# Kernel tuning notes

Measured on AMD Instinct MI355X. Metric: run time of the kernel, lower is better.

Reference implementation:

```python
import jax, jax.numpy as jnp
import numpy as np
import math

D_MODEL = 1024
N_HEADS = 16
D_HEAD = D_MODEL // N_HEADS
EPS = 1e-5


def layer_norm(x, w, b):
    mu = jnp.mean(x, axis=-1, keepdims=True)
    var = jnp.mean(jnp.square(x - mu), axis=-1, keepdims=True)
    return (x - mu) * jax.lax.rsqrt(var + EPS) * w + b


def setup_inputs() -> dict:
    key = jax.random.key(0)
    ks = jax.random.split(key, 8)
    b, n, d = 1, 4096, D_MODEL
    s = 0.02
    return {
        "x": jax.random.normal(ks[0], (b, n, d), dtype=jnp.float32),
        "ln1_w": jnp.ones((d,), jnp.float32),
        "ln1_b": jnp.zeros((d,), jnp.float32),
        "ln2_w": jnp.ones((d,), jnp.float32),
        "ln2_b": jnp.zeros((d,), jnp.float32),
        "w_qkv": jax.random.normal(ks[1], (d, 3 * d), jnp.float32) * s,  # [in, out]
        "w_o": jax.random.normal(ks[2], (d, d), jnp.float32) * s,
        "w_ff1": jax.random.normal(ks[3], (d, 4 * d), jnp.float32) * s,
        "b_ff1": jnp.zeros((4 * d,), jnp.float32),
        "w_ff2": jax.random.normal(ks[4], (4 * d, d), jnp.float32) * s,
        "b_ff2": jnp.zeros((d,), jnp.float32),
    }


def reference(x, ln1_w, ln1_b, ln2_w, ln2_b, w_qkv, w_o, w_ff1, b_ff1, w_ff2, b_ff2):
    b, n, d = x.shape
    # --- attention sub-block ---
    h = layer_norm(x, ln1_w, ln1_b)
    qkv = (h @ w_qkv).reshape(b, n, 3, N_HEADS, D_HEAD)
    q, k, v = qkv[:, :, 0], qkv[:, :, 1], qkv[:, :, 2]  # [b, n, h, dh]
    scale = 1.0 / math.sqrt(D_HEAD)
    s = jnp.einsum("bqhd,bkhd->bhqk", q, k) * scale  # materialized [b,h,n,n]
    causal = jnp.tril(jnp.ones((n, n), dtype=bool))
    s = jnp.where(causal, s, -jnp.inf)
    a = jax.nn.softmax(s, axis=-1)
    out = jnp.einsum("bhqk,bkhd->bqhd", a, v).reshape(b, n, d)
    x = x + out @ w_o
    # --- FFN sub-block ---
    h2 = layer_norm(x, ln2_w, ln2_b)
    ff = jax.nn.gelu(h2 @ w_ff1 + b_ff1, approximate=False) @ w_ff2 + b_ff2
    return x + ff
```

## Files before the change

kernel.cpp:

```cpp
#include <hip/hip_runtime.h>
#include <hip/hip_bf16.h>
#include <cstdint>
#include <cstddef>

typedef __attribute__((ext_vector_type(8))) __bf16 bf16x8;
typedef __attribute__((ext_vector_type(4))) __bf16 bf16x4;
typedef __attribute__((ext_vector_type(4))) float f32x4;
typedef __attribute__((ext_vector_type(16))) float f32x16;
typedef __attribute__((ext_vector_type(4))) unsigned int uint4v;

#define MFMA16(a, b, c) __builtin_amdgcn_mfma_f32_16x16x32_bf16(a, b, c, 0, 0, 0)
#define MFMA32(a, b, c) __builtin_amdgcn_mfma_f32_32x32x16_bf16(a, b, c, 0, 0, 0)

__device__ __forceinline__ void gload_lds16(const void* g, void* l) {
  __builtin_amdgcn_global_load_lds(
      (__attribute__((address_space(1))) uint32_t*)g,
      (__attribute__((address_space(3))) uint32_t*)l,
      16, 0, 0);
}

__device__ __forceinline__ unsigned pkbf(float a, float b) {
  unsigned short x = __builtin_bit_cast(unsigned short, (__bf16)a);
  unsigned short y = __builtin_bit_cast(unsigned short, (__bf16)b);
  return (unsigned)x | ((unsigned)y << 16);
}

__device__ __forceinline__ float fexp2(float x) {
  float r;
  asm("v_exp_f32 %0, %1" : "=v"(r) : "v"(x));
  return r;
}

__global__ __launch_bounds__(256) void pre_kernel(
    const float* __restrict__ w_qkv, __bf16* __restrict__ wqkvT,
    const float* __restrict__ x, const float* __restrict__ ln1_w,
    const float* __restrict__ ln1_b, __bf16* __restrict__ h) {
  __shared__ float sm[32 * 33];
  int bid = blockIdx.x;
  int tx = threadIdx.x, ty = threadIdx.y;
  if (bid < 3072) {
    int bx = bid % 96, by = bid / 96;
    int gcol = bx * 32 + tx;
#pragma unroll
    for (int j = 0; j < 4; j++) {
      int grow = by * 32 + ty + j * 8;
      sm[(ty + j * 8) * 33 + tx] = w_qkv[(size_t)grow * 3072 + gcol];
    }
    __syncthreads();
#pragma unroll
    for (int j = 0; j < 4; j++) {
      int n = bx * 32 + ty + j * 8;
      wqkvT[(size_t)n * 1024 + by * 32 + tx] = (__bf16)sm[tx * 33 + ty + j * 8];
    }
    return;
  }
  int row = bid - 3072;
  int t = ty * 32 + tx;
  const float4* xr = (const float4*)(x + (size_t)row * 1024);
  float4 v = xr[t];
  float s = v.x + v.y + v.z + v.w;
  float sq = v.x * v.x + v.y * v.y + v.z * v.z + v.w * v.w;
#pragma unroll
  for (int m = 1; m < 64; m <<= 1) {
    s += __shfl_xor(s, m);
    sq += __shfl_xor(sq, m);
  }
  float* rs = sm;
  float* rq = sm + 4;
  int wid = t >> 6;
  if ((t & 63) == 0) { rs[wid] = s; rq[wid] = sq; }
  __syncthreads();
  s = rs[0] + rs[1] + rs[2] + rs[3];
  sq = rq[0] + rq[1] + rq[2] + rq[3];
  float mean = s * (1.0f / 1024.0f);
  float var = sq * (1.0f / 1024.0f) - mean * mean;
  float rstd = rsqrtf(var + 1e-5f);
  float4 wv = ((const float4*)ln1_w)[t];
  float4 bv = ((const float4*)ln1_b)[t];
  bf16x4 o;
  o[0] = (__bf16)((v.x - mean) * rstd * wv.x + bv.x);
  o[1] = (__bf16)((v.y - mean) * rstd * wv.y + bv.y);
  o[2] = (__bf16)((v.z - mean) * rstd * wv.z + bv.z);
  o[3] = (__bf16)((v.w - mean) * rstd * wv.w + bv.w);
  *(bf16x4*)(h + (size_t)row * 1024 + t * 4) = o;
}

__global__ __launch_bounds__(256, 2) void gemm_splitk128_kernel(
    const __bf16* __restrict__ A, const __bf16* __restrict__ BT,
    int M, int N, int K, int kchunk, __bf16* __restrict__ P) {
  __shared__ __bf16 lsA[128 * 64];
  __shared__ __bf16 lsB[128 * 64];
  int t = threadIdx.x;
  int m0 = blockIdx.y * 128, n0 = blockIdx.x * 128;
  int kbase = blockIdx.z * kchunk;
  __bf16* pout = P + (size_t)blockIdx.z * M * N;
  int wid = t >> 6, lane = t & 63, lo = lane & 15, g = lane >> 4;
  int wr = wid >> 1, wc = wid & 1;
  f32x4 acc[4][4] = {};
  const __bf16* ag = A + (size_t)(m0 + (t >> 3)) * K + (t & 7) * 8;
  const __bf16* bg = BT + (size_t)(n0 + (t >> 3)) * K + (t & 7) * 8;
  for (int k0 = kbase; k0 < kbase + kchunk; k0 += 64) {
#pragma unroll
    for (int i = 0; i < 4; i++) {
      gload_lds16(ag + (size_t)i * 32 * K + k0, &lsA[i * 2048 + t * 8]);
      gload_lds16(bg + (size_t)i * 32 * K + k0, &lsB[i * 2048 + t * 8]);
    }
    __syncthreads();
#pragma unroll
    for (int kk = 0; kk < 2; kk++) {
      bf16x8 af[4], bfr[4];
#pragma unroll
      for (int mi = 0; mi < 4; mi++)
        af[mi] = *(const bf16x8*)&lsA[(wr * 64 + mi * 16 + lo) * 64 + kk * 32 + g * 8];
#pragma unroll
      for (int ni = 0; ni < 4; ni++)
        bfr[ni] = *(const bf16x8*)&lsB[(wc * 64 + ni * 16 + lo) * 64 + kk * 32 + g * 8];
#pragma unroll
      for (int mi = 0; mi < 4; mi++)
#pragma unroll
        for (int ni = 0; ni < 4; ni++)
          acc[mi][ni] = MFMA16(af[mi], bfr[ni], acc[mi][ni]);
    }
    __syncthreads();
  }
#pragma unroll
  for (int mi = 0; mi < 4; mi++) {
#pragma unroll
    for (int ni = 0; ni < 4; ni++) {
      int col = n0 + wc * 64 + ni * 16 + lo;
      int row0 = m0 + wr * 64 + mi * 16 + g * 4;
#pragma unroll
      for (int r = 0; r < 4; r++)
        pout[(size_t)(row0 + r) * N + col] = (__bf16)acc[mi][ni][r];
    }
  }
}

__global__ __launch_bounds__(256) void out_reduce_ln_kernel(
    const __bf16* __restrict__ p0, const __bf16* __restrict__ p1,
    const float* __restrict__ x, const float* __restrict__ w,
    const float* __restrict__ b, float* __restrict__ x2,
    __bf16* __restrict__ h) {
  int row = blockIdx.x, t = threadIdx.x;
  size_t base = (size_t)row * 1024 + t * 4;
  bf16x4 a = *(const bf16x4*)&p0[base];
  bf16x4 b4 = *(const bf16x4*)&p1[base];
  float4 xv = *(const float4*)&x[base];
  float4 v;
  v.x = xv.x + (float)a[0] + (float)b4[0];
  v.y = xv.y + (float)a[1] + (float)b4[1];
  v.z = xv.z + (float)a[2] + (float)b4[2];
  v.w = xv.w + (float)a[3] + (float)b4[3];
  *(float4*)&x2[base] = v;
  float s = v.x + v.y + v.z + v.w;
  float sq = v.x * v.x + v.y * v.y + v.z * v.z + v.w * v.w;
#pragma unroll
  for (int m = 1; m < 64; m <<= 1) {
    s += __shfl_xor(s, m);
    sq += __shfl_xor(sq, m);
  }
  __shared__ float rs[4], rq[4];
  int wid = t >> 6;
  if ((t & 63) == 0) { rs[wid] = s; rq[wid] = sq; }
  __syncthreads();
  s = rs[0] + rs[1] + rs[2] + rs[3];
  sq = rq[0] + rq[1] + rq[2] + rq[3];
  float mean = s * (1.0f / 1024.0f);
  float var = sq * (1.0f / 1024.0f) - mean * mean;
  float rstd = rsqrtf(var + 1e-5f);
  float4 wv = ((const float4*)w)[t];
  float4 bv = ((const float4*)b)[t];
  bf16x4 o;
  o[0] = (__bf16)((v.x - mean) * rstd * wv.x + bv.x);
  o[1] = (__bf16)((v.y - mean) * rstd * wv.y + bv.y);
  o[2] = (__bf16)((v.z - mean) * rstd * wv.z + bv.z);
  o[3] = (__bf16)((v.w - mean) * rstd * wv.w + bv.w);
  *(bf16x4*)&h[base] = o;
}

template <int EPI>
__global__ __launch_bounds__(512, 2) void gemm256_kernel(
    const __bf16* __restrict__ A, const __bf16* __restrict__ BT,
    int M, int N, int K, int nkc,
    const float* __restrict__ bias, __bf16* __restrict__ outb,
    __bf16* __restrict__ P0, __bf16* __restrict__ P1,
    __bf16* __restrict__ P2, __bf16* __restrict__ P3) {
  __shared__ __bf16 lsA[2][2][128 * 64];
  __shared__ __bf16 lsB[2][2][128 * 64];
  int nbx = N >> 8;
  int nwg = (M >> 8) * nbx;
  int bid = blockIdx.x;
  int swz = (bid & 7) * (nwg >> 3) + (bid >> 3);
  int m0 = (swz / nbx) << 8, n0 = (swz % nbx) << 8;
  int kc = blockIdx.y;
  int kt0 = kc * nkc;
  int t = threadIdx.x;
  int wid = t >> 6, lane = t & 63, lo = lane & 15, g = lane >> 4;
  int wm = wid >> 2, wn = wid & 3;
  int srow = t >> 3, sgrp = t & 7;

  auto stA = [&](int d, int h, int kt) {
#pragma unroll
    for (int i = 0; i < 2; i++) {
      int row = i * 64 + srow;
      int gs = (sgrp ^ (row & 7)) * 8;
      gload_lds16(A + (size_t)(m0 + h * 128 + row) * K + kt * 64 + gs,
                  &lsA[d][h][(i * 512 + t) * 8]);
    }
  };
  auto stB = [&](int d, int h, int kt) {
#pragma unroll
    for (int i = 0; i < 2; i++) {
      int row = i * 64 + srow;
      int gs = (sgrp ^ (row & 7)) * 8;
      gload_lds16(BT + (size_t)(n0 + h * 128 + row) * K + kt * 64 + gs,
                  &lsB[d][h][(i * 512 + t) * 8]);
    }
  };
  auto rdA = [&](int d, int f, int kk) -> bf16x8 {
    int row = (f & 3) * 32 + wm * 16 + lo;
    return *(const bf16x8*)&lsA[d][f >> 2][row * 64 + (((kk * 4 + g) ^ (lo & 7)) * 8)];
  };
  auto rdB = [&](int d, int ni, int kk) -> bf16x8 {
    int row = (ni & 1) * 64 + wn * 16 + lo;
    return *(const bf16x8*)&lsB[d][ni >> 1][row * 64 + (((kk * 4 + g) ^ (lo & 7)) * 8)];
  };

  f32x4 acc[8][4] = {};
  stA(0, 0, kt0); stB(0, 0, kt0); stB(0, 1, kt0); stA(0, 1, kt0);
  asm volatile("s_waitcnt vmcnt(4)" ::: "memory");
  __builtin_amdgcn_s_barrier();

  for (int ki = 0; ki < nkc; ki++) {
    int kt = kt0 + ki;
    int d = ki & 1, nx = d ^ 1;
    bool pf = (ki + 1) < nkc;
    bf16x8 fa[4][2], fb0[2][2], fb1[2][2];
#pragma unroll
    for (int f = 0; f < 4; f++) { fa[f][0] = rdA(d, f, 0); fa[f][1] = rdA(d, f, 1); }
#pragma unroll
    for (int n = 0; n < 2; n++) { fb0[n][0] = rdB(d, n, 0); fb0[n][1] = rdB(d, n, 1); }
    if (pf) { stA(nx, 0, kt + 1); stB(nx, 0, kt + 1); }
    __builtin_amdgcn_s_barrier();
    __builtin_amdgcn_s_setprio(1);
#pragma unroll
    for (int f = 0; f < 4; f++)
#pragma unroll
      for (int n = 0; n < 2; n++) {
        acc[f][n] = MFMA16(fa[f][0], fb0[n][0], acc[f][n]);
        acc[f][n] = MFMA16(fa[f][1], fb0[n][1], acc[f][n]);
      }
    __builtin_amdgcn_s_setprio(0);
    asm volatile("s_waitcnt vmcnt(6)" ::: "memory");
    __builtin_amdgcn_s_barrier();
#pragma unroll
    for (int n = 0; n < 2; n++) { fb1[n][0] = rdB(d, 2 + n, 0); fb1[n][1] = rdB(d, 2 + n, 1); }
    if (pf) stB(nx, 1, kt + 1);
    __builtin_amdgcn_s_barrier();
    __builtin_amdgcn_s_setprio(1);
#pragma unroll
    for (int f = 0; f < 4; f++)
#pragma unroll
      for (int n = 0; n < 2; n++) {
        acc[f][2 + n] = MFMA16(fa[f][0], fb1[n][0], acc[f][2 + n]);
        acc[f][2 + n] = MFMA16(fa[f][1], fb1[n][1], acc[f][2 + n]);
      }
    __builtin_amdgcn_s_setprio(0);
    asm volatile("s_waitcnt vmcnt(6)" ::: "memory");
    __builtin_amdgcn_s_barrier();
#pragma unroll
    for (int f = 0; f < 4; f++) { fa[f][0] = rdA(d, 4 + f, 0); fa[f][1] = rdA(d, 4 + f, 1); }
    if (pf) stA(nx, 1, kt + 1);
    __builtin_amdgcn_s_barrier();
    __builtin_amdgcn_s_setprio(1);
#pragma unroll
    for (int f = 0; f < 4; f++)
#pragma unroll
      for (int n = 0; n < 2; n++) {
        acc[4 + f][2 + n] = MFMA16(fa[f][0], fb1[n][0], acc[4 + f][2 + n]);
        acc[4 + f][2 + n] = MFMA16(fa[f][1], fb1[n][1], acc[4 + f][2 + n]);
      }
    __builtin_amdgcn_s_setprio(0);
    __builtin_amdgcn_s_barrier();
    __builtin_amdgcn_s_setprio(1);
#pragma unroll
    for (int f = 0; f < 4; f++)
#pragma unroll
      for (int n = 0; n < 2; n++) {
        acc[4 + f][n] = MFMA16(fa[f][0], fb0[n][0], acc[4 + f][n]);
        acc[4 + f][n] = MFMA16(fa[f][1], fb0[n][1], acc[4 + f][n]);
      }
    __builtin_amdgcn_s_setprio(0);
    asm volatile("s_waitcnt vmcnt(4)" ::: "memory");
    __builtin_amdgcn_s_barrier();
  }

  __bf16* pk = (EPI == 4) ? ((kc == 0) ? P0 : (kc == 1) ? P1 : (kc == 2) ? P2 : P3)
                          : nullptr;
#pragma unroll
  for (int f = 0; f < 8; f++) {
    int row0 = m0 + (f >> 2) * 128 + (f & 3) * 32 + wm * 16 + g * 4;
#pragma unroll
    for (int ni = 0; ni < 4; ni++) {
      int col = n0 + (ni >> 1) * 128 + (ni & 1) * 64 + wn * 16 + lo;
      if (EPI == 0) {
        int sE = col >> 10, rem = col & 1023, hh = rem >> 6, dd = rem & 63;
        if (sE < 2) {
          float qs = (sE == 0) ? 0.1803368801111204f : 1.0f;
#pragma unroll
          for (int r = 0; r < 4; r++)
            outb[((size_t)(sE * 16 + hh) * 4096 + row0 + r) * 64 + dd] =
                (__bf16)(acc[f][ni][r] * qs);
        } else {
          bf16x4 pk4;
#pragma unroll
          for (int r = 0; r < 4; r++) pk4[r] = (__bf16)acc[f][ni][r];
          *(bf16x4*)&outb[(size_t)32 * 4096 * 64 + ((size_t)(hh * 64 + dd)) * 4096 + row0] = pk4;
        }
      } else if (EPI == 2) {
        float bv = bias[col];
#pragma unroll
        for (int r = 0; r < 4; r++) {
          float vv = acc[f][ni][r] + bv;
          float gg = 0.5f * vv * (1.0f + erff(vv * 0.70710678118f));
          outb[(size_t)(row0 + r) * N + col] = (__bf16)gg;
        }
      } else {
#pragma unroll
        for (int r = 0; r < 4; r++)
          pk[(size_t)(row0 + r) * N + col] = (__bf16)acc[f][ni][r];
      }
    }
  }
}

__global__ __launch_bounds__(256) void ff2_reduce_kernel(
    const __bf16* __restrict__ p0, const __bf16* __restrict__ p1,
    const __bf16* __restrict__ p2, const __bf16* __restrict__ p3,
    const float* __restrict__ x2, const float* __restrict__ bias,
    float* __restrict__ out) {
  size_t i8 = ((size_t)blockIdx.x * 256 + threadIdx.x) * 8;
  bf16x8 a = *(const bf16x8*)&p0[i8];
  bf16x8 b = *(const bf16x8*)&p1[i8];
  bf16x8 c = *(const bf16x8*)&p2[i8];
  bf16x8 d = *(const bf16x8*)&p3[i8];
  int col = (int)(i8 & 1023);
  float4 xa = *(const float4*)&x2[i8];
  float4 xb = *(const float4*)&x2[i8 + 4];
  float4 ba = *(const float4*)&bias[col];
  float4 bb = *(const float4*)&bias[col + 4];
  float4 oa, ob;
  oa.x = xa.x + ba.x + (float)a[0] + (float)b[0] + (float)c[0] + (float)d[0];
  oa.y = xa.y + ba.y + (float)a[1] + (float)b[1] + (float)c[1] + (float)d[1];
  oa.z = xa.z + ba.z + (float)a[2] + (float)b[2] + (float)c[2] + (float)d[2];
  oa.w = xa.w + ba.w + (float)a[3] + (float)b[3] + (float)c[3] + (float)d[3];
  ob.x = xb.x + bb.x + (float)a[4] + (float)b[4] + (float)c[4] + (float)d[4];
  ob.y = xb.y + bb.y + (float)a[5] + (float)b[5] + (float)c[5] + (float)d[5];
  ob.z = xb.z + bb.z + (float)a[6] + (float)b[6] + (float)c[6] + (float)d[6];
  ob.w = xb.w + bb.w + (float)a[7] + (float)b[7] + (float)c[7] + (float)d[7];
  *(float4*)&out[i8] = oa;
  *(float4*)&out[i8 + 4] = ob;
}

__global__ __launch_bounds__(512, 4) void attn_fused_kernel(
    const __bf16* __restrict__ Q, const __bf16* __restrict__ Kb,
    const __bf16* __restrict__ VTb, __bf16* __restrict__ O,
    const float* __restrict__ w_o, __bf16* __restrict__ woT,
    const float* __restrict__ w_ff1, __bf16* __restrict__ wff1T,
    const float* __restrict__ w_ff2, __bf16* __restrict__ wff2T) {
  constexpr int NSEQ = 4096;
  __shared__ __bf16 lds[2][2][2][64 * 64];
  int orig = blockIdx.x;
  int t = threadIdx.x;

  if (orig >= 512) {
    int b = orig - 512;
    const float* in; __bf16* outw; int K, N, bx, by;
    if (b < 1024)      { in = w_o;   outw = woT;   K = 1024; N = 1024; bx = b & 31;  by = b >> 5; }
    else if (b < 5120) { int c = b - 1024; in = w_ff1; outw = wff1T; K = 1024; N = 4096; bx = c & 127; by = c >> 7; }
    else               { int c = b - 5120; in = w_ff2; outw = wff2T; K = 4096; N = 1024; bx = c & 31;  by = c >> 5; }
    float* tile = (float*)lds;
    int tx = t & 31, ty = t >> 5;
#pragma unroll
    for (int j = 0; j < 2; j++) {
      int r = ty + j * 16;
      tile[r * 33 + tx] = in[(size_t)(by * 32 + r) * N + bx * 32 + tx];
    }
    __syncthreads();
#pragma unroll
    for (int j = 0; j < 2; j++) {
      int r = ty + j * 16;
      outw[(size_t)(bx * 32 + r) * K + by * 32 + tx] = (__bf16)tile[tx * 33 + r];
    }
    return;
  }

  int xcd = orig & 7, rank = orig >> 3;
  int hv = rank >> 5;
  int hd2 = (rank >> 4) & 1;
  int itr = rank & 15;
  int head = xcd * 2 + hd2;
  int it = hv ? itr : (31 - itr);
  int wid = t >> 6, lane = t & 63;
  int lo = lane & 31, hi = lane >> 5;
  int qsub = wid & 3, kpar = wid >> 2;
  const __bf16* kh = Kb + (size_t)head * NSEQ * 64;
  const __bf16* vth = VTb + (size_t)head * 64 * NSEQ;
  int qlow = it * 128 + qsub * 32;
  int qrow = qlow + lo;
  const __bf16* qh = Q + (size_t)head * NSEQ * 64 + (size_t)qrow * 64;
  bf16x8 bq[4];
#pragma unroll
  for (int c = 0; c < 4; c++) bq[c] = *(const bf16x8*)(qh + c * 16 + hi * 8);

  const unsigned onesu = 0x3F803F80u;
  uint4v onev = {onesu, onesu, onesu, onesu};
  bf16x8 vones = __builtin_bit_cast(bf16x8, onev);

  f32x16 acc0 = {}, acc1 = {};
  f32x16 lacc = {};
  int srow = t >> 3;
  int sgs = ((t & 7) ^ (srow & 7)) * 8;

  int off[4];
#pragma unroll
  for (int c = 0; c < 4; c++) off[c] = lo * 64 + (((c * 2 + hi) ^ (lo & 7)) * 8);
  const __bf16* lk0 = &lds[0][kpar][0][0];
  const __bf16* lk1 = &lds[1][kpar][0][0];
  const __bf16* lv0 = &lds[0][kpar][1][0];
  const __bf16* lv1 = &lds[1][kpar][1][0];
  const __bf16* khs = kh + srow * 64 + sgs;
  const __bf16* vts = vth + (size_t)srow * NSEQ + sgs;

  auto stage_tile = [&](int d, int par, int kt) {
    gload_lds16(khs + (size_t)kt * 4096, &lds[d][par][0][t * 8]);
    gload_lds16(vts + kt * 64, &lds[d][par][1][t * 8]);
  };

  int ns = it + 1;
  int qtop = qlow + 31;
  stage_tile(0, 0, 0);
  stage_tile(0, 1, 1);
  __syncthreads();

#define ATTN_STEP(CUR)                                                         \
  {                                                                            \
    if (j + 1 < ns) {                                                          \
      stage_tile((CUR) ^ 1, 0, 2 * j + 2);                                     \
      stage_tile((CUR) ^ 1, 1, 2 * j + 3);                                     \
    }                                                                          \
    int kt = 2 * j + kpar;                                                     \
    if (kt * 64 <= qtop) {                                                     \
      const __bf16* lk = (CUR) ? lk1 : lk0;                                    \
      const __bf16* lvt = (CUR) ? lv1 : lv0;                                   \
      f32x16 s0 = {}, s1 = {};                                                 \
      __builtin_amdgcn_s_setprio(1);                                           \
      _Pragma("unroll") for (int c = 0; c < 4; c++) {                          \
        bf16x8 ka0 = *(const bf16x8*)&lk[off[c]];                              \
        bf16x8 ka1 = *(const bf16x8*)&lk[2048 + off[c]];                       \
        s0 = MFMA32(ka0, bq[c], s0);                                           \
        s1 = MFMA32(ka1, bq[c], s1);                                           \
      }                                                                        \
      __builtin_amdgcn_s_setprio(0);                                           \
      if (kt * 64 + 63 > qlow) {                                               \
        _Pragma("unroll") for (int i = 0; i < 16; i++) {                       \
          int key0 = kt * 64 + (i & 3) + 8 * (i >> 2) + 4 * hi;                \
          if (key0 > qrow) s0[i] = -3.0e38f;                                   \
          if (key0 + 32 > qrow) s1[i] = -3.0e38f;                              \
        }                                                                      \
      }                                                                        \
      _Pragma("unroll") for (int i = 0; i < 16; i++) {                         \
        s0[i] = fexp2(s0[i]);                                                  \
        s1[i] = fexp2(s1[i]);                                                  \
      }                                                                        \
      uint4v pw[4];                                                            \
      _Pragma("unroll") for (int b = 0; b < 2; b++) {                          \
        int off2 = b * 8;                                                      \
        unsigned a0 = pkbf(s0[off2 + 0], s0[off2 + 1]);                        \
        unsigned a1 = pkbf(s0[off2 + 2], s0[off2 + 3]);                        \
        unsigned b0 = pkbf(s0[off2 + 4], s0[off2 + 5]);                        \
        unsigned b1 = pkbf(s0[off2 + 6], s0[off2 + 7]);                        \
        asm("v_permlane32_swap_b32 %0, %1" : "+v"(a0), "+v"(b0));              \
        asm("v_permlane32_swap_b32 %0, %1" : "+v"(a1), "+v"(b1));              \
        pw[b][0] = a0; pw[b][1] = a1; pw[b][2] = b0; pw[b][3] = b1;            \
        unsigned c0 = pkbf(s1[off2 + 0], s1[off2 + 1]);                        \
        unsigned c1 = pkbf(s1[off2 + 2], s1[off2 + 3]);                        \
        unsigned d0 = pkbf(s1[off2 + 4], s1[off2 + 5]);                        \
        unsigned d1 = pkbf(s1[off2 + 6], s1[off2 + 7]);                        \
        asm("v_permlane32_swap_b32 %0, %1" : "+v"(c0), "+v"(d0));              \
        asm("v_permlane32_swap_b32 %0, %1" : "+v"(c1), "+v"(d1));              \
        pw[2 + b][0] = c0; pw[2 + b][1] = c1; pw[2 + b][2] = d0;               \
        pw[2 + b][3] = d1;                                                     \
      }                                                                        \
      __builtin_amdgcn_s_setprio(1);                                           \
      _Pragma("unroll") for (int b = 0; b < 4; b++) {                          \
        bf16x8 pf = __builtin_bit_cast(bf16x8, pw[b]);                         \
        bf16x8 va0 = *(const bf16x8*)&lvt[off[b]];                             \
        bf16x8 va1 = *(const bf16x8*)&lvt[2048 + off[b]];                      \
        acc0 = MFMA32(va0, pf, acc0);                                          \
        acc1 = MFMA32(va1, pf, acc1);                                          \
        lacc = MFMA32(vones, pf, lacc);                                        \
      }                                                                        \
      __builtin_amdgcn_s_setprio(0);                                           \
    }                                                                          \
    __syncthreads();                                                           \
  }

  int j = 0;
  for (;;) {
    ATTN_STEP(0);
    if (++j >= ns) break;
    ATTN_STEP(1);
    if (++j >= ns) break;
  }
#undef ATTN_STEP

  float* fl = (float*)lds;
  float* lbuf = fl;
  float* ab = fl + 256;
  __bf16* bounce = (__bf16*)(fl + 256 + 9216);
  if (kpar == 1) {
    lbuf[qsub * 64 + lane] = lacc[0];
    int base = (qsub * 64 + lane) * 36;
#pragma unroll
    for (int k2 = 0; k2 < 16; k2 += 4) {
      float4 v0; v0.x = acc0[k2]; v0.y = acc0[k2 + 1]; v0.z = acc0[k2 + 2]; v0.w = acc0[k2 + 3];
      *(float4*)&ab[base + k2] = v0;
      float4 v1; v1.x = acc1[k2]; v1.y = acc1[k2 + 1]; v1.z = acc1[k2 + 2]; v1.w = acc1[k2 + 3];
      *(float4*)&ab[base + 16 + k2] = v1;
    }
  }
  __syncthreads();
  if (kpar == 0) {
    float lsum = lacc[0] + lbuf[qsub * 64 + lane];
    float linv = 1.0f / lsum;
    int base = (qsub * 64 + lane) * 36;
    f32x16 b0, b1;
#pragma unroll
    for (int k2 = 0; k2 < 16; k2 += 4) {
      float4 v0 = *(float4*)&ab[base + k2];
      b0[k2] = v0.x; b0[k2 + 1] = v0.y; b0[k2 + 2] = v0.z; b0[k2 + 3] = v0.w;
      float4 v1 = *(float4*)&ab[base + 16 + k2];
      b1[k2] = v1.x; b1[k2 + 1] = v1.y; b1[k2 + 2] = v1.z; b1[k2 + 3] = v1.w;
    }
    __bf16* region = bounce + qsub * 2048;
#pragma unroll
    for (int dt = 0; dt < 2; dt++) {
#pragma unroll
      for (int rp = 0; rp < 8; rp++) {
        int r = rp * 2;
        float a0 = dt ? acc1[r] : acc0[r], a1 = dt ? acc1[r + 1] : acc0[r + 1];
        float c0 = dt ? b1[r] : b0[r], c1 = dt ? b1[r + 1] : b0[r + 1];
        float e0 = (a0 + c0) * linv;
        float e1 = (a1 + c1) * linv;
        int d = dt * 32 + (r & 3) + 8 * (r >> 2) + 4 * hi;
        int bytecol = d * 2;
        int g16 = bytecol >> 4, rem16 = bytecol & 15;
        *(unsigned*)((char*)region + lo * 128 + ((g16 ^ (lo & 7)) * 16 + rem16)) = pkbf(e0, e1);
      }
    }
#pragma unroll
    for (int j2 = 0; j2 < 4; j2++) {
      int idx = j2 * 64 + lane;
      int row = idx >> 3, g = idx & 7;
      bf16x8 v = *(const bf16x8*)((char*)region + row * 128 + ((g ^ (row & 7)) * 16));
      *(bf16x8*)&O[(size_t)(it * 128 + qsub * 32 + row) * 1024 + head * 64 + g * 8] = v;
    }
  }
}

extern "C" void kernel_launch(void* const* d_in, const int* in_sizes, int n_in,
                              void* d_out, int out_size, void* d_ws, size_t ws_size,
                              hipStream_t stream) {
  const float* x = (const float*)d_in[0];
  const float* ln1_w = (const float*)d_in[1];
  const float* ln1_b = (const float*)d_in[2];
  const float* ln2_w = (const float*)d_in[3];
  const float* ln2_b = (const float*)d_in[4];
  const float* w_qkv = (const float*)d_in[5];
  const float* w_o = (const float*)d_in[6];
  const float* w_ff1 = (const float*)d_in[7];
  const float* b_ff1 = (const float*)d_in[8];
  const float* w_ff2 = (const float*)d_in[9];
  const float* b_ff2 = (const float*)d_in[10];
  float* out = (float*)d_out;

  const size_t D = 1024, NT = 4096;
  __bf16* wqkvT = (__bf16*)d_ws;
  __bf16* woT = wqkvT + 3072 * D;
  __bf16* wff1T = woT + D * D;
  __bf16* wff2T = wff1T + 4096 * D;
  __bf16* hbuf = wff2T + D * 4096;
  __bf16* qkvb = hbuf + NT * D;
  __bf16* attnb = qkvb + 3 * NT * D;
  __bf16* a1 = qkvb;
  float* x2 = (float*)(attnb + NT * D);
  __bf16* p0 = (__bf16*)d_ws;
  __bf16* p1 = p0 + NT * D;
  __bf16* p2 = hbuf;
  __bf16* p3 = (__bf16*)(x2 + NT * D);
  __bf16* pA = qkvb;
  __bf16* pB = pA + NT * D;

  dim3 tb(32, 8);
  pre_kernel<<<3072 + 4096, tb, 0, stream>>>(w_qkv, wqkvT, x, ln1_w, ln1_b, hbuf);
  gemm256_kernel<0><<<192, 512, 0, stream>>>(hbuf, wqkvT, 4096, 3072, 1024, 16,
                                             nullptr, qkvb, nullptr, nullptr, nullptr, nullptr);
  attn_fused_kernel<<<512 + 9216, 512, 0, stream>>>(
      qkvb, qkvb + 16 * NT * 64, qkvb + 32 * NT * 64, attnb,
      w_o, woT, w_ff1, wff1T, w_ff2, wff2T);
  gemm_splitk128_kernel<<<dim3(8, 32, 2), 256, 0, stream>>>(
      attnb, woT, 4096, 1024, 1024, 512, pA);
  out_reduce_ln_kernel<<<4096, 256, 0, stream>>>(pA, pB, x, ln2_w, ln2_b, x2, hbuf);
  gemm256_kernel<2><<<256, 512, 0, stream>>>(hbuf, wff1T, 4096, 4096, 1024, 16,
                                             b_ff1, a1, nullptr, nullptr, nullptr, nullptr);
  gemm256_kernel<4><<<dim3(64, 4), 512, 0, stream>>>(a1, wff2T, 4096, 1024, 4096, 16,
                                                     nullptr, nullptr, p0, p1, p2, p3);
  ff2_reduce_kernel<<<2048, 256, 0, stream>>>(p0, p1, p2, p3, x2, b_ff2, out);
}
```

Baseline: 228.2 us.

## Split attention key-parity halves into separate blocks with merge kernel

Attention work that was split across two wave groups inside one 512-thread block (even/odd key tiles) now runs as separate 256-thread blocks, each writing unnormalized partial outputs and row sums to workspace. A new merge kernel adds the two partials and normalizes them into the attention output. This drops the in-block LDS reduction and halves LDS per block, giving more and smaller blocks for better occupancy and scheduling. The cost is an extra kernel launch, the extra global traffic for the partials, and bf16 rounding of the partials before they are summed.

```diff
diff --git a/kernel.cpp b/kernel.cpp
--- a/kernel.cpp
+++ b/kernel.cpp
@@ -362,19 +362,40 @@
   *(float4*)&out[i8 + 4] = ob;
 }
 
-__global__ __launch_bounds__(512, 4) void attn_fused_kernel(
+__global__ __launch_bounds__(256) void attn_merge_kernel(
+    const __bf16* __restrict__ pO, const float* __restrict__ pL,
+    __bf16* __restrict__ attnb) {
+  size_t i8 = ((size_t)blockIdx.x * 256 + threadIdx.x) * 8;
+  int row = (int)(i8 >> 10);
+  int col = (int)(i8 & 1023);
+  int head = col >> 6, d = col & 63;
+  size_t po_off = (((size_t)head * 4096) + row) * 64 + d;
+  bf16x8 a = *(const bf16x8*)&pO[po_off];
+  bf16x8 b = *(const bf16x8*)&pO[(size_t)16 * 4096 * 64 + po_off];
+  float l0 = pL[(size_t)head * 4096 + row];
+  float l1 = pL[(size_t)16 * 4096 + (size_t)head * 4096 + row];
+  float linv = 1.0f / (l0 + l1);
+  bf16x8 o;
+#pragma unroll
+  for (int i = 0; i < 8; i++)
+    o[i] = (__bf16)(((float)a[i] + (float)b[i]) * linv);
+  *(bf16x8*)&attnb[i8] = o;
+}
+
+__global__ __launch_bounds__(256, 4) void attn_fused_kernel(
     const __bf16* __restrict__ Q, const __bf16* __restrict__ Kb,
-    const __bf16* __restrict__ VTb, __bf16* __restrict__ O,
+    const __bf16* __restrict__ VTb, __bf16* __restrict__ pO,
+    float* __restrict__ pL,
     const float* __restrict__ w_o, __bf16* __restrict__ woT,
     const float* __restrict__ w_ff1, __bf16* __restrict__ wff1T,
     const float* __restrict__ w_ff2, __bf16* __restrict__ wff2T) {
   constexpr int NSEQ = 4096;
-  __shared__ __bf16 lds[2][2][2][64 * 64];
+  __shared__ __bf16 lds[2][2][64 * 64];
   int orig = blockIdx.x;
   int t = threadIdx.x;
 
-  if (orig >= 512) {
-    int b = orig - 512;
+  if (orig >= 1024) {
+    int b = orig - 1024;
     const float* in; __bf16* outw; int K, N, bx, by;
     if (b < 1024)      { in = w_o;   outw = woT;   K = 1024; N = 1024; bx = b & 31;  by = b >> 5; }
     else if (b < 5120) { int c = b - 1024; in = w_ff1; outw = wff1T; K = 1024; N = 4096; bx = c & 127; by = c >> 7; }
@@ -382,32 +403,35 @@
     float* tile = (float*)lds;
     int tx = t & 31, ty = t >> 5;
 #pragma unroll
-    for (int j = 0; j < 2; j++) {
-      int r = ty + j * 16;
+    for (int j = 0; j < 4; j++) {
+      int r = ty + j * 8;
       tile[r * 33 + tx] = in[(size_t)(by * 32 + r) * N + bx * 32 + tx];
     }
     __syncthreads();
 #pragma unroll
-    for (int j = 0; j < 2; j++) {
-      int r = ty + j * 16;
+    for (int j = 0; j < 4; j++) {
+      int r = ty + j * 8;
       outw[(size_t)(bx * 32 + r) * K + by * 32 + tx] = (__bf16)tile[tx * 33 + r];
     }
     return;
   }
 
-  int xcd = orig & 7, rank = orig >> 3;
-  int hv = rank >> 5;
-  int hd2 = (rank >> 4) & 1;
-  int itr = rank & 15;
+  int xcd = orig & 7, r = orig >> 3;
+  int kpar = r & 1;
+  int r2 = r >> 1;
+  int hv = r2 >> 5;
+  int hd2 = (r2 >> 4) & 1;
+  int itr = r2 & 15;
   int head = xcd * 2 + hd2;
   int it = hv ? itr : (31 - itr);
   int wid = t >> 6, lane = t & 63;
   int lo = lane & 31, hi = lane >> 5;
-  int qsub = wid & 3, kpar = wid >> 2;
+  int qsub = wid;
   const __bf16* kh = Kb + (size_t)head * NSEQ * 64;
   const __bf16* vth = VTb + (size_t)head * 64 * NSEQ;
   int qlow = it * 128 + qsub * 32;
   int qrow = qlow + lo;
+  int qtop = qlow + 31;
   const __bf16* qh = Q + (size_t)head * NSEQ * 64 + (size_t)qrow * 64;
   bf16x8 bq[4];
 #pragma unroll
@@ -425,31 +449,29 @@
   int off[4];
 #pragma unroll
   for (int c = 0; c < 4; c++) off[c] = lo * 64 + (((c * 2 + hi) ^ (lo & 7)) * 8);
-  const __bf16* lk0 = &lds[0][kpar][0][0];
-  const __bf16* lk1 = &lds[1][kpar][0][0];
-  const __bf16* lv0 = &lds[0][kpar][1][0];
-  const __bf16* lv1 = &lds[1][kpar][1][0];
+  const __bf16* lk0 = &lds[0][0][0];
+  const __bf16* lk1 = &lds[1][0][0];
+  const __bf16* lv0 = &lds[0][1][0];
+  const __bf16* lv1 = &lds[1][1][0];
   const __bf16* khs = kh + srow * 64 + sgs;
   const __bf16* vts = vth + (size_t)srow * NSEQ + sgs;
 
-  auto stage_tile = [&](int d, int par, int kt) {
-    gload_lds16(khs + (size_t)kt * 4096, &lds[d][par][0][t * 8]);
-    gload_lds16(vts + kt * 64, &lds[d][par][1][t * 8]);
+  auto stage_tile = [&](int d, int kt) {
+#pragma unroll
+    for (int i = 0; i < 2; i++) {
+      gload_lds16(khs + (size_t)kt * 4096 + i * 2048, &lds[d][0][i * 2048 + t * 8]);
+      gload_lds16(vts + (size_t)i * 32 * NSEQ + kt * 64, &lds[d][1][i * 2048 + t * 8]);
+    }
   };
 
   int ns = it + 1;
-  int qtop = qlow + 31;
-  stage_tile(0, 0, 0);
-  stage_tile(0, 1, 1);
+  stage_tile(0, kpar);
   __syncthreads();
 
 #define ATTN_STEP(CUR)                                                         \
   {                                                                            \
-    if (j + 1 < ns) {                                                          \
-      stage_tile((CUR) ^ 1, 0, 2 * j + 2);                                     \
-      stage_tile((CUR) ^ 1, 1, 2 * j + 3);                                     \
-    }                                                                          \
     int kt = 2 * j + kpar;                                                     \
+    if (j + 1 < ns) stage_tile((CUR) ^ 1, kt + 2);                             \
     if (kt * 64 <= qtop) {                                                     \
       const __bf16* lk = (CUR) ? lk1 : lk0;                                    \
       const __bf16* lvt = (CUR) ? lv1 : lv0;                                   \
@@ -515,57 +537,30 @@
   }
 #undef ATTN_STEP
 
-  float* fl = (float*)lds;
-  float* lbuf = fl;
-  float* ab = fl + 256;
-  __bf16* bounce = (__bf16*)(fl + 256 + 9216);
-  if (kpar == 1) {
-    lbuf[qsub * 64 + lane] = lacc[0];
-    int base = (qsub * 64 + lane) * 36;
-#pragma unroll
-    for (int k2 = 0; k2 < 16; k2 += 4) {
-      float4 v0; v0.x = acc0[k2]; v0.y = acc0[k2 + 1]; v0.z = acc0[k2 + 2]; v0.w = acc0[k2 + 3];
-      *(float4*)&ab[base + k2] = v0;
-      float4 v1; v1.x = acc1[k2]; v1.y = acc1[k2 + 1]; v1.z = acc1[k2 + 2]; v1.w = acc1[k2 + 3];
-      *(float4*)&ab[base + 16 + k2] = v1;
+  if (hi == 0) pL[((size_t)kpar * 16 + head) * 4096 + qlow + lo] = lacc[0];
+  __bf16* bounce = (__bf16*)lds;
+  __bf16* region = bounce + qsub * 2048;
+#pragma unroll
+  for (int dt = 0; dt < 2; dt++) {
+#pragma unroll
+    for (int rp = 0; rp < 8; rp++) {
+      int rr = rp * 2;
+      float e0 = dt ? acc1[rr] : acc0[rr];
+      float e1 = dt ? acc1[rr + 1] : acc0[rr + 1];
+      int d = dt * 32 + (rr & 3) + 8 * (rr >> 2) + 4 * hi;
+      int bytecol = d * 2;
+      int g16 = bytecol >> 4, rem16 = bytecol & 15;
+      *(unsigned*)((char*)region + lo * 128 + ((g16 ^ (lo & 7)) * 16 + rem16)) = pkbf(e0, e1);
     }
   }
   __syncthreads();
-  if (kpar == 0) {
-    float lsum = lacc[0] + lbuf[qsub * 64 + lane];
-    float linv = 1.0f / lsum;
-    int base = (qsub * 64 + lane) * 36;
-    f32x16 b0, b1;
-#pragma unroll
-    for (int k2 = 0; k2 < 16; k2 += 4) {
-      float4 v0 = *(float4*)&ab[base + k2];
-      b0[k2] = v0.x; b0[k2 + 1] = v0.y; b0[k2 + 2] = v0.z; b0[k2 + 3] = v0.w;
-      float4 v1 = *(float4*)&ab[base + 16 + k2];
-      b1[k2] = v1.x; b1[k2 + 1] = v1.y; b1[k2 + 2] = v1.z; b1[k2 + 3] = v1.w;
-    }
-    __bf16* region = bounce + qsub * 2048;
-#pragma unroll
-    for (int dt = 0; dt < 2; dt++) {
-#pragma unroll
-      for (int rp = 0; rp < 8; rp++) {
-        int r = rp * 2;
-        float a0 = dt ? acc1[r] : acc0[r], a1 = dt ? acc1[r + 1] : acc0[r + 1];
-        float c0 = dt ? b1[r] : b0[r], c1 = dt ? b1[r + 1] : b0[r + 1];
-        float e0 = (a0 + c0) * linv;
-        float e1 = (a1 + c1) * linv;
-        int d = dt * 32 + (r & 3) + 8 * (r >> 2) + 4 * hi;
-        int bytecol = d * 2;
-        int g16 = bytecol >> 4, rem16 = bytecol & 15;
-        *(unsigned*)((char*)region + lo * 128 + ((g16 ^ (lo & 7)) * 16 + rem16)) = pkbf(e0, e1);
-      }
-    }
-#pragma unroll
-    for (int j2 = 0; j2 < 4; j2++) {
-      int idx = j2 * 64 + lane;
-      int row = idx >> 3, g = idx & 7;
-      bf16x8 v = *(const bf16x8*)((char*)region + row * 128 + ((g ^ (row & 7)) * 16));
-      *(bf16x8*)&O[(size_t)(it * 128 + qsub * 32 + row) * 1024 + head * 64 + g * 8] = v;
-    }
+  __bf16* pok = pO + (size_t)kpar * 16 * 4096 * 64 + (((size_t)head * 4096) + qlow) * 64;
+#pragma unroll
+  for (int j2 = 0; j2 < 4; j2++) {
+    int idx = j2 * 64 + lane;
+    int row = idx >> 3, g = idx & 7;
+    bf16x8 v = *(const bf16x8*)((char*)region + row * 128 + ((g ^ (row & 7)) * 16));
+    *(bf16x8*)&pok[(size_t)row * 64 + g * 8] = v;
   }
 }
 
@@ -601,14 +596,17 @@
   __bf16* p3 = (__bf16*)(x2 + NT * D);
   __bf16* pA = qkvb;
   __bf16* pB = pA + NT * D;
+  __bf16* pOb = (__bf16*)x2;
+  float* pLb = (float*)p3;
 
   dim3 tb(32, 8);
   pre_kernel<<<3072 + 4096, tb, 0, stream>>>(w_qkv, wqkvT, x, ln1_w, ln1_b, hbuf);
   gemm256_kernel<0><<<192, 512, 0, stream>>>(hbuf, wqkvT, 4096, 3072, 1024, 16,
                                              nullptr, qkvb, nullptr, nullptr, nullptr, nullptr);
-  attn_fused_kernel<<<512 + 9216, 512, 0, stream>>>(
-      qkvb, qkvb + 16 * NT * 64, qkvb + 32 * NT * 64, attnb,
+  attn_fused_kernel<<<1024 + 9216, 256, 0, stream>>>(
+      qkvb, qkvb + 16 * NT * 64, qkvb + 32 * NT * 64, pOb, pLb,
       w_o, woT, w_ff1, wff1T, w_ff2, wff2T);
+  attn_merge_kernel<<<2048, 256, 0, stream>>>(pOb, pLb, attnb);
   gemm_splitk128_kernel<<<dim3(8, 32, 2), 256, 0, stream>>>(
       attnb, woT, 4096, 1024, 1024, 512, pA);
   out_reduce_ln_kernel<<<4096, 256, 0, stream>>>(pA, pB, x, ln2_w, ln2_b, x2, hbuf);
```

Result: no change. 231.9 us (+1.6%).
